# Kernel tuning notes

Hardware: AMD Instinct MI355X
Metric: run time of the kernel (lower is better)

## Reference

```python
import jax, jax.numpy as jnp
import numpy as np

B, S, H = 512, 50, 20
N_NODE, N_CAT = 100000, 1298
MEM, CLUS = 20, 10
STEP, KBLOCKS = 1, 2
MIX = 0.52  # a = 0.52*attn_last + 0.48*ht


def setup_inputs() -> dict:
    key = jax.random.key(0)
    ks = iter(jax.random.split(key, 48))
    stdv = 1.0 / np.sqrt(H)
    def u(shape):
        return jax.random.uniform(next(ks), shape, jnp.float32, -stdv, stdv)
    inp = {}
    inp['inputs'] = jax.random.randint(next(ks), (B, S), 0, N_NODE, dtype=jnp.int32)
    inp['category'] = jax.random.randint(next(ks), (B, S), 0, N_CAT, dtype=jnp.int32)
    inp['A'] = jax.random.uniform(next(ks), (B, S, 2 * S), jnp.float32)
    inp['mask'] = jnp.ones((B, S), jnp.int32)
    # embeddings
    inp['emb'] = u((N_NODE, H)); inp['emb1'] = u((N_CAT, H))
    # GNN params
    inp['w_ih'] = u((3 * H, 2 * H)); inp['w_hh'] = u((3 * H, H))
    inp['b_ih'] = u((3 * H,)); inp['b_hh'] = u((3 * H,))
    inp['b_iah'] = u((H,)); inp['b_oah'] = u((H,))
    inp['w_ein'] = u((H, H)); inp['b_ein'] = u((H,))
    inp['w_eout'] = u((H, H)); inp['b_eout'] = u((H,))
    # two single-head MHAs
    for p in ('mha', 'mha1'):
        inp[p + '_in_w'] = u((3 * H, H)); inp[p + '_in_b'] = u((3 * H,))
        inp[p + '_out_w'] = u((H, H)); inp[p + '_out_b'] = u((H,))
    # residual blocks
    for p in ('rn', 'rn1'):
        inp[p + '_w1'] = u((H, H)); inp[p + '_b1'] = u((H,))
        inp[p + '_w2'] = u((H, H)); inp[p + '_b2'] = u((H,))
    # memory readout
    inp['mem_M'] = u((CLUS, MEM)); inp['mem_Wa'] = u((2 * H, MEM)); inp['mem_fc'] = u((MEM, MEM))
    # heads
    inp['wc'] = u((H, 3 * H)); inp['bc'] = u((H,))
    inp['wp'] = u((H, 3 * H)); inp['bp'] = u((H,))
    return inp


def _mha(x, w_in, b_in, w_out, b_out):
    # Faithful to torch nn.MultiheadAttention (seq-first, 1 head):
    # x is [B,S,H] but torch treats dim0 as sequence -> attention mixes along axis 0.
    E = x.shape[-1]
    q, k, v = jnp.split(x @ w_in.T + b_in, 3, axis=-1)
    q = q * (1.0 / jnp.sqrt(jnp.float32(E)))
    scores = jnp.einsum('lne,mne->nlm', q, k)        # [S_axis1, L, L]
    attn = jax.nn.softmax(scores, axis=-1)
    out = jnp.einsum('nlm,mne->lne', attn, v)
    return out @ w_out.T + b_out


def _residual(x, w1, b1, w2, b2):
    # eval mode: dropout = identity
    return x + jax.nn.relu(x @ w1.T + b1) @ w2.T + b2


def _gnn_cell(A, h, w_ein, b_ein, w_eout, b_eout, b_iah, b_oah, w_ih, b_ih, w_hh, b_hh):
    s = h.shape[1]
    inp_in = jnp.einsum('bij,bjh->bih', A[:, :, :s], h @ w_ein.T + b_ein) + b_iah
    inp_out = jnp.einsum('bij,bjh->bih', A[:, :, s:2 * s], h @ w_eout.T + b_eout) + b_oah
    gi = jnp.concatenate([inp_in, inp_out], -1) @ w_ih.T + b_ih
    gh = h @ w_hh.T + b_hh
    i_r, i_i, i_n = jnp.split(gi, 3, -1)
    h_r, h_i, h_n = jnp.split(gh, 3, -1)
    r = jax.nn.sigmoid(i_r + h_r)
    z = jax.nn.sigmoid(i_i + h_i)
    n = jnp.tanh(i_n + r * h_n)
    return n + z * (h - n)


def reference(inputs, category, A, mask, emb, emb1, w_ih, w_hh, b_ih, b_hh, b_iah, b_oah,
              w_ein, b_ein, w_eout, b_eout,
              mha_in_w, mha_in_b, mha_out_w, mha_out_b,
              mha1_in_w, mha1_in_b, mha1_out_w, mha1_out_b,
              rn_w1, rn_b1, rn_w2, rn_b2, rn1_w1, rn1_b1, rn1_w2, rn1_b2,
              mem_M, mem_Wa, mem_fc, wc, bc, wp, bp):
    item_h = emb[inputs]          # [B,S,H]
    cat_h = emb1[category]        # [B,S,H]
    for _ in range(STEP):
        item_h = _gnn_cell(A, item_h, w_ein, b_ein, w_eout, b_eout,
                           b_iah, b_oah, w_ih, b_ih, w_hh, b_hh)
    bidx = jnp.arange(mask.shape[0])
    last = jnp.sum(mask, 1) - 1
    ht_item = item_h[bidx, last]
    ht_cat = cat_h[bidx, last]
    x = item_h
    for _ in range(KBLOCKS):
        x = _residual(_mha(x, mha_in_w, mha_in_b, mha_out_w, mha_out_b), rn_w1, rn_b1, rn_w2, rn_b2)
    a_item = MIX * x[bidx, last] + (1 - MIX) * ht_item
    y = cat_h
    for _ in range(KBLOCKS):
        y = _residual(_mha(y, mha1_in_w, mha1_in_b, mha1_out_w, mha1_out_b), rn1_w1, rn1_b1, rn1_w2, rn1_b2)
    a_cat = MIX * y[bidx, last] + (1 - MIX) * ht_cat
    a = jnp.concatenate([a_item, a_cat], -1)                # [B, 2H]
    att = jax.nn.softmax((a @ mem_Wa) @ mem_M.T, axis=-1)   # [B, CLUS]
    reps = jnp.tanh((att @ mem_M) @ mem_fc)                 # [B, MEM]
    car = jnp.concatenate([a, reps], -1)                    # [B, 3H]
    final = jax.nn.sigmoid(car @ wc.T + bc) * (car @ wp.T + bp)
    scores = final @ emb[1:].T                              # [B, N_NODE-1]
    return scores
```

## Files before the change

### kernel.cpp

```cpp
#include <hip/hip_runtime.h>
#include <hip/hip_bf16.h>

#define BB 512
#define SS 50
#define HH 20
#define NN 100000
#define MC 128
#define MT 16
#define PBSTRIDE ((size_t)BB*24)

__device__ __forceinline__ float frcp(float x){
#if __has_builtin(__builtin_amdgcn_rcpf)
  return __builtin_amdgcn_rcpf(x);
#else
  return 1.f/x;
#endif
}
__device__ __forceinline__ float fsig(float x){ return frcp(1.f + __expf(-x)); }
__device__ __forceinline__ float ftanh(float x){ return 1.f - 2.f*frcp(1.f + __expf(2.f*x)); }

__global__ __launch_bounds__(256)
void k_gnnqkv(const int* __restrict__ inputs, const int* __restrict__ category,
              const float* __restrict__ A, const int* __restrict__ mask,
              const float* __restrict__ emb, const float* __restrict__ emb1,
              const float* __restrict__ w_ih, const float* __restrict__ w_hh,
              const float* __restrict__ b_ih, const float* __restrict__ b_hh,
              const float* __restrict__ b_iah, const float* __restrict__ b_oah,
              const float* __restrict__ w_ein, const float* __restrict__ b_ein,
              const float* __restrict__ w_eout, const float* __restrict__ b_eout,
              const float* __restrict__ inw0, const float* __restrict__ inb0,
              const float* __restrict__ inw1, const float* __restrict__ inb1,
              float* __restrict__ q_t, float* __restrict__ k_t, float* __restrict__ v_t,
              int* __restrict__ last, float* __restrict__ ht_item, float* __restrict__ ht_cat)
{
    __shared__ float sA[SS*2*SS];
    __shared__ float sit[SS*HH], sct[SS*HH], shin[SS*HH], shout[SS*HH];
    __shared__ float sinp[SS*HH], soutp[SS*HH];
    __shared__ float swein[HH*HH], sweout[HH*HH];
    __shared__ float swih[60*40], swhh[60*HH];
    __shared__ float sw0[60*HH], sw1w[60*HH];
    __shared__ float sbein[HH], sbeout[HH], sbih[60], sbhh[60], sbiah[HH], sboah[HH], sb0[60], sb1b[60];
    __shared__ int slast;
    const int b = blockIdx.x, t = threadIdx.x;

    for (int i=t;i<SS*2*SS;i+=256) sA[i] = A[(size_t)b*SS*2*SS + i];
    for (int i=t;i<HH*HH;i+=256) { swein[i]=w_ein[i]; sweout[i]=w_eout[i]; }
    for (int i=t;i<60*40;i+=256) swih[i]=w_ih[i];
    for (int i=t;i<60*HH;i+=256) { swhh[i]=w_hh[i]; sw0[i]=inw0[i]; sw1w[i]=inw1[i]; }
    if (t<60){ sbih[t]=b_ih[t]; sbhh[t]=b_hh[t]; sb0[t]=inb0[t]; sb1b[t]=inb1[t]; }
    if (t<HH){ sbein[t]=b_ein[t]; sbeout[t]=b_eout[t]; sbiah[t]=b_iah[t]; sboah[t]=b_oah[t]; }
    for (int i=t;i<SS*HH;i+=256){
        int r=i/HH, e=i%HH;
        sit[i]=emb [(size_t)inputs  [b*SS+r]*HH+e];
        sct[i]=emb1[(size_t)category[b*SS+r]*HH+e];
    }
    if (t==0){ int s=0; for (int j=0;j<SS;j++) s+=mask[b*SS+j]; slast=s-1; }
    __syncthreads();

    for (int i=t;i<SS*HH;i+=256){
        int r=i/HH, c=i%HH;
        float si=sbein[c], so=sbeout[c];
        #pragma unroll
        for (int e=0;e<HH;e++){ float hv=sit[r*HH+e]; si+=swein[c*HH+e]*hv; so+=sweout[c*HH+e]*hv; }
        shin[i]=si; shout[i]=so;
    }
    __syncthreads();
    for (int i=t;i<SS*HH;i+=256){
        int r=i/HH, e=i%HH;
        float ai=sbiah[e], ao=sboah[e];
        for (int j=0;j<SS;j++){
            ai+=sA[r*2*SS+j]   *shin [j*HH+e];
            ao+=sA[r*2*SS+SS+j]*shout[j*HH+e];
        }
        sinp[i]=ai; soutp[i]=ao;
    }
    __syncthreads();
    float nh[4];
    #pragma unroll
    for (int ii=0;ii<4;ii++){
        int i=t+ii*256;
        if (i<SS*HH){
            int r=i/HH, e=i%HH;
            float gir=sbih[e], gii=sbih[20+e], gin=sbih[40+e];
            #pragma unroll
            for (int k=0;k<HH;k++){
                float vi=sinp[r*HH+k], vo=soutp[r*HH+k];
                gir+=swih[e*40+k]*vi      + swih[e*40+HH+k]*vo;
                gii+=swih[(20+e)*40+k]*vi + swih[(20+e)*40+HH+k]*vo;
                gin+=swih[(40+e)*40+k]*vi + swih[(40+e)*40+HH+k]*vo;
            }
            float ghr=sbhh[e], ghi=sbhh[20+e], ghn=sbhh[40+e];
            #pragma unroll
            for (int k=0;k<HH;k++){
                float hv=sit[r*HH+k];
                ghr+=swhh[e*HH+k]*hv; ghi+=swhh[(20+e)*HH+k]*hv; ghn+=swhh[(40+e)*HH+k]*hv;
            }
            float rr=fsig(gir+ghr), zz=fsig(gii+ghi);
            float nn2=ftanh(gin+rr*ghn);
            nh[ii]=nn2+zz*(sit[i]-nn2);
        }
    }
    __syncthreads();
    #pragma unroll
    for (int ii=0;ii<4;ii++){ int i=t+ii*256; if (i<SS*HH) sit[i]=nh[ii]; }
    __syncthreads();

    if (t<HH)                    ht_item[b*HH+t]      = sit[slast*HH+t];
    else if (t>=32 && t<32+HH)   ht_cat [b*HH+(t-32)] = sct[slast*HH+(t-32)];
    else if (t==63)              last[b]=slast;

    const float SCALE = 0.22360679774997896f;
    for (int oi=t; oi<2*SS*60; oi+=256){
        int p=oi/(SS*60); int rem=oi%(SS*60); int r=rem/60; int c=rem%60;
        const float* src = p? sct  : sit;
        const float* w   = p? sw1w : sw0;
        const float* bb_ = p? sb1b : sb0;
        float acc=bb_[c];
        #pragma unroll
        for (int e=0;e<HH;e++) acc += w[c*HH+e]*src[r*HH+e];
        int which=c/HH, cc=c%HH;
        size_t off=((size_t)(p*SS+r)*BB + b)*HH + cc;
        if (which==0)      q_t[off]=acc*SCALE;
        else if (which==1) k_t[off]=acc;
        else               v_t[off]=acc;
    }
}

__global__ __launch_bounds__(256)
void k_attn(const float* __restrict__ q_t, const float* __restrict__ k_t,
            const float* __restrict__ v_t, float* __restrict__ pbuf)
{
    __shared__ float sk[MC*HH], sv[MC*HH];
    const int n=blockIdx.x, p=blockIdx.y, mc=blockIdx.z, t=threadIdx.x;
    const size_t base=(size_t)(p*SS+n)*BB;
    {
        const float4* kb=(const float4*)(k_t+(base+(size_t)mc*MC)*HH);
        const float4* vb=(const float4*)(v_t+(base+(size_t)mc*MC)*HH);
        float4* sk4=(float4*)sk; float4* sv4=(float4*)sv;
        for (int i=t;i<MC*HH/4;i+=256){ sk4[i]=kb[i]; sv4[i]=vb[i]; }
    }
    __syncthreads();
    float4 q0[5], q1[5];
    {
        const float4* qp0=(const float4*)(q_t+(base+t)*HH);
        const float4* qp1=(const float4*)(q_t+(base+t+256)*HH);
        #pragma unroll
        for (int i=0;i<5;i++){ q0[i]=qp0[i]; q1[i]=qp1[i]; }
    }
    float4 o0[5], o1[5];
    #pragma unroll
    for (int i=0;i<5;i++){ o0[i]=make_float4(0.f,0.f,0.f,0.f); o1[i]=make_float4(0.f,0.f,0.f,0.f); }
    float mx0=-1e30f, mx1=-1e30f, sm0=0.f, sm1=0.f;

    for (int mt0=0; mt0<MC; mt0+=MT){
        float s0[MT], s1[MT];
        float tm0=-1e30f, tm1=-1e30f;
        #pragma unroll
        for (int j=0;j<MT;j++){
            const float4* kr=(const float4*)(sk+(mt0+j)*HH);
            float a0=0.f, a1=0.f;
            #pragma unroll
            for (int i=0;i<5;i++){
                float4 kv=kr[i];
                a0+=q0[i].x*kv.x+q0[i].y*kv.y+q0[i].z*kv.z+q0[i].w*kv.w;
                a1+=q1[i].x*kv.x+q1[i].y*kv.y+q1[i].z*kv.z+q1[i].w*kv.w;
            }
            s0[j]=a0; s1[j]=a1;
            tm0=fmaxf(tm0,a0); tm1=fmaxf(tm1,a1);
        }
        float nm0=fmaxf(mx0,tm0), nm1=fmaxf(mx1,tm1);
        float c0=__expf(mx0-nm0), c1=__expf(mx1-nm1);
        sm0*=c0; sm1*=c1;
        #pragma unroll
        for (int i=0;i<5;i++){
            o0[i].x*=c0; o0[i].y*=c0; o0[i].z*=c0; o0[i].w*=c0;
            o1[i].x*=c1; o1[i].y*=c1; o1[i].z*=c1; o1[i].w*=c1;
        }
        mx0=nm0; mx1=nm1;
        #pragma unroll
        for (int j=0;j<MT;j++){
            float p0=__expf(s0[j]-nm0), p1=__expf(s1[j]-nm1);
            sm0+=p0; sm1+=p1;
            const float4* vr=(const float4*)(sv+(mt0+j)*HH);
            #pragma unroll
            for (int i=0;i<5;i++){
                float4 vv=vr[i];
                o0[i].x+=p0*vv.x; o0[i].y+=p0*vv.y; o0[i].z+=p0*vv.z; o0[i].w+=p0*vv.w;
                o1[i].x+=p1*vv.x; o1[i].y+=p1*vv.y; o1[i].z+=p1*vv.z; o1[i].w+=p1*vv.w;
            }
        }
    }
    float* pb0 = pbuf + (((size_t)(p*SS+n)*4+mc)*BB + t)*24;
    float4* w0=(float4*)pb0;
    w0[0]=make_float4(mx0,sm0,o0[0].x,o0[0].y);
    w0[1]=make_float4(o0[0].z,o0[0].w,o0[1].x,o0[1].y);
    w0[2]=make_float4(o0[1].z,o0[1].w,o0[2].x,o0[2].y);
    w0[3]=make_float4(o0[2].z,o0[2].w,o0[3].x,o0[3].y);
    w0[4]=make_float4(o0[3].z,o0[3].w,o0[4].x,o0[4].y);
    w0[5]=make_float4(o0[4].z,o0[4].w,0.f,0.f);
    float4* w1=(float4*)(pb0 + (size_t)256*24);
    w1[0]=make_float4(mx1,sm1,o1[0].x,o1[0].y);
    w1[1]=make_float4(o1[0].z,o1[0].w,o1[1].x,o1[1].y);
    w1[2]=make_float4(o1[1].z,o1[1].w,o1[2].x,o1[2].y);
    w1[3]=make_float4(o1[2].z,o1[2].w,o1[3].x,o1[3].y);
    w1[4]=make_float4(o1[3].z,o1[3].w,o1[4].x,o1[4].y);
    w1[5]=make_float4(o1[4].z,o1[4].w,0.f,0.f);
}

__device__ __forceinline__ void merge_res(const float* __restrict__ pbase,
    const float* __restrict__ sow, const float* __restrict__ sob,
    const float* __restrict__ sw1, const float* __restrict__ sb1,
    const float* __restrict__ sw2, const float* __restrict__ sb2,
    float* __restrict__ xo)
{
    float mx=-1e30f;
    #pragma unroll
    for (int mc2=0;mc2<4;mc2++) mx=fmaxf(mx, pbase[mc2*PBSTRIDE]);
    float sum=0.f, o[HH];
    #pragma unroll
    for (int e=0;e<HH;e++) o[e]=0.f;
    #pragma unroll
    for (int mc2=0;mc2<4;mc2++){
        const float4* pc=(const float4*)(pbase+mc2*PBSTRIDE);
        float4 a=pc[0], b4=pc[1], c4=pc[2], d4=pc[3], e4=pc[4], f4=pc[5];
        float cc=__expf(a.x-mx);
        sum+=a.y*cc;
        o[0]+=a.z*cc;  o[1]+=a.w*cc;
        o[2]+=b4.x*cc; o[3]+=b4.y*cc; o[4]+=b4.z*cc; o[5]+=b4.w*cc;
        o[6]+=c4.x*cc; o[7]+=c4.y*cc; o[8]+=c4.z*cc; o[9]+=c4.w*cc;
        o[10]+=d4.x*cc; o[11]+=d4.y*cc; o[12]+=d4.z*cc; o[13]+=d4.w*cc;
        o[14]+=e4.x*cc; o[15]+=e4.y*cc; o[16]+=e4.z*cc; o[17]+=e4.w*cc;
        o[18]+=f4.x*cc; o[19]+=f4.y*cc;
    }
    float inv=frcp(sum);
    float ao[HH];
    #pragma unroll
    for (int e=0;e<HH;e++) ao[e]=o[e]*inv;
    float mo[HH];
    #pragma unroll
    for (int e=0;e<HH;e++){
        float acc=sob[e];
        #pragma unroll
        for (int f=0;f<HH;f++) acc+=sow[e*HH+f]*ao[f];
        mo[e]=acc;
    }
    float u[HH];
    #pragma unroll
    for (int g=0;g<HH;g++){
        float acc=sb1[g];
        #pragma unroll
        for (int f=0;f<HH;f++) acc+=sw1[g*HH+f]*mo[f];
        u[g]=fmaxf(acc,0.f);
    }
    #pragma unroll
    for (int e=0;e<HH;e++){
        float acc=mo[e]+sb2[e];
        #pragma unroll
        for (int g=0;g<HH;g++) acc+=sw2[e*HH+g]*u[g];
        xo[e]=acc;
    }
}

__global__ __launch_bounds__(256)
void k_finqkv(const float* __restrict__ pbuf,
    const float* __restrict__ ow0, const float* __restrict__ ob0,
    const float* __restrict__ w10, const float* __restrict__ b10,
    const float* __restrict__ w20, const float* __restrict__ b20,
    const float* __restrict__ iw0, const float* __restrict__ ib0,
    const float* __restrict__ ow1, const float* __restrict__ ob1,
    const float* __restrict__ w11, const float* __restrict__ b11,
    const float* __restrict__ w21, const float* __restrict__ b21,
    const float* __restrict__ iw1, const float* __restrict__ ib1,
    float* __restrict__ q_t, float* __restrict__ k_t, float* __restrict__ v_t)
{
    __shared__ float sow[400], sw1[400], sw2[400], siw[1200];
    __shared__ float sob[20], sb1[20], sb2[20], sib[60];
    const int p=blockIdx.y, t=threadIdx.x;
    const int s=blockIdx.x>>1, b=(blockIdx.x&1)*256+t;
    const float* OW=p?ow1:ow0; const float* OB=p?ob1:ob0;
    const float* W1=p?w11:w10; const float* B1=p?b11:b10;
    const float* W2=p?w21:w20; const float* B2=p?b21:b20;
    const float* IW=p?iw1:iw0; const float* IB=p?ib1:ib0;
    for (int i=t;i<400;i+=256){ sow[i]=OW[i]; sw1[i]=W1[i]; sw2[i]=W2[i]; }
    for (int i=t;i<1200;i+=256) siw[i]=IW[i];
    if (t<20){ sob[t]=OB[t]; sb1[t]=B1[t]; sb2[t]=B2[t]; }
    if (t<60) sib[t]=IB[t];
    __syncthreads();
    const float* pbase = pbuf + (((size_t)(p*SS+s)*4)*BB + b)*24;
    float xo[HH];
    merge_res(pbase, sow,sob,sw1,sb1,sw2,sb2, xo);
    const float SCALE = 0.22360679774997896f;
    size_t off0=((size_t)(p*SS+s)*BB + b)*HH;
    #pragma unroll
    for (int c=0;c<HH;c++){
        float aq=sib[c], ak=sib[20+c], av=sib[40+c];
        #pragma unroll
        for (int e=0;e<HH;e++){ float xv=xo[e]; aq+=siw[c*HH+e]*xv; ak+=siw[(20+c)*HH+e]*xv; av+=siw[(40+c)*HH+e]*xv; }
        q_t[off0+c]=aq*SCALE; k_t[off0+c]=ak; v_t[off0+c]=av;
    }
}

__global__ __launch_bounds__(256)
void k_fin(const float* __restrict__ pbuf,
    const float* __restrict__ ow0, const float* __restrict__ ob0,
    const float* __restrict__ w10, const float* __restrict__ b10,
    const float* __restrict__ w20, const float* __restrict__ b20,
    const float* __restrict__ ow1, const float* __restrict__ ob1,
    const float* __restrict__ w11, const float* __restrict__ b11,
    const float* __restrict__ w21, const float* __restrict__ b21,
    float* __restrict__ xout)
{
    __shared__ float sow[400], sw1[400], sw2[400];
    __shared__ float sob[20], sb1[20], sb2[20];
    const int p=blockIdx.y, t=threadIdx.x;
    const int s=blockIdx.x>>1, b=(blockIdx.x&1)*256+t;
    const float* OW=p?ow1:ow0; const float* OB=p?ob1:ob0;
    const float* W1=p?w11:w10; const float* B1=p?b11:b10;
    const float* W2=p?w21:w20; const float* B2=p?b21:b20;
    for (int i=t;i<400;i+=256){ sow[i]=OW[i]; sw1[i]=W1[i]; sw2[i]=W2[i]; }
    if (t<20){ sob[t]=OB[t]; sb1[t]=B1[t]; sb2[t]=B2[t]; }
    __syncthreads();
    const float* pbase = pbuf + (((size_t)(p*SS+s)*4)*BB + b)*24;
    float xo[HH];
    merge_res(pbase, sow,sob,sw1,sb1,sw2,sb2, xo);
    size_t off=((size_t)(p*BB+b)*SS + s)*HH;
    #pragma unroll
    for (int e=0;e<HH;e++) xout[off+e]=xo[e];
}

__global__ __launch_bounds__(64)
void k_head(const float* __restrict__ xout, const int* __restrict__ last,
            const float* __restrict__ ht_item, const float* __restrict__ ht_cat,
            const float* __restrict__ mem_M, const float* __restrict__ mem_Wa,
            const float* __restrict__ mem_fc,
            const float* __restrict__ wc, const float* __restrict__ bc,
            const float* __restrict__ wp, const float* __restrict__ bp,
            float* __restrict__ final_)
{
    int b=blockIdx.x*64+threadIdx.x;
    if (b>=BB) return;
    int l=last[b];
    const float* xi = xout + ((size_t)(0*BB+b)*SS + l)*HH;
    const float* xc = xout + ((size_t)(1*BB+b)*SS + l)*HH;
    float a[40];
    #pragma unroll
    for (int e=0;e<HH;e++){
        a[e]    = 0.52f*xi[e] + 0.48f*ht_item[b*HH+e];
        a[20+e] = 0.52f*xc[e] + 0.48f*ht_cat [b*HH+e];
    }
    float t20[20];
    #pragma unroll
    for (int j=0;j<20;j++){
        float acc=0.f;
        #pragma unroll
        for (int k=0;k<40;k++) acc+=a[k]*mem_Wa[k*20+j];
        t20[j]=acc;
    }
    float lg[10]; float mxv=-1e30f;
    #pragma unroll
    for (int c=0;c<10;c++){
        float acc=0.f;
        #pragma unroll
        for (int j=0;j<20;j++) acc+=t20[j]*mem_M[c*20+j];
        lg[c]=acc; mxv=fmaxf(mxv,acc);
    }
    float se=0.f;
    #pragma unroll
    for (int c=0;c<10;c++){ lg[c]=__expf(lg[c]-mxv); se+=lg[c]; }
    float inv=frcp(se);
    #pragma unroll
    for (int c=0;c<10;c++) lg[c]*=inv;
    float am[20];
    #pragma unroll
    for (int j=0;j<20;j++){
        float acc=0.f;
        #pragma unroll
        for (int c=0;c<10;c++) acc+=lg[c]*mem_M[c*20+j];
        am[j]=acc;
    }
    float reps[20];
    #pragma unroll
    for (int j2=0;j2<20;j2++){
        float acc=0.f;
        #pragma unroll
        for (int j=0;j<20;j++) acc+=am[j]*mem_fc[j*20+j2];
        reps[j2]=ftanh(acc);
    }
    #pragma unroll
    for (int e=0;e<HH;e++){
        float c1=bc[e], c2=bp[e];
        #pragma unroll
        for (int k=0;k<40;k++){ c1+=a[k]*wc[e*60+k]; c2+=a[k]*wp[e*60+k]; }
        #pragma unroll
        for (int k=0;k<20;k++){ c1+=reps[k]*wc[e*60+40+k]; c2+=reps[k]*wp[e*60+40+k]; }
        final_[b*HH+e]=fsig(c1)*c2;
    }
}

__global__ __launch_bounds__(256)
void k_scores(const float* __restrict__ final_, const float* __restrict__ emb,
              float* __restrict__ out)
{
    int node = blockIdx.x*256 + threadIdx.x;
    if (node >= NN-1) return;
    float4 er[5];
    const float4* e4 = (const float4*)(emb + ((size_t)node + 1)*HH);
    #pragma unroll
    for (int i=0;i<5;i++) er[i]=e4[i];
    float* op = out + node;
    for (int b = 0; b < BB; b++) {
        const float4* fb = (const float4*)(final_ + b*HH);
        float acc = 0.f;
        #pragma unroll
        for (int i=0;i<5;i++){
            float4 f=fb[i];
            acc += f.x*er[i].x + f.y*er[i].y + f.z*er[i].z + f.w*er[i].w;
        }
        *op = acc;
        op += (NN-1);
    }
}

extern "C" void kernel_launch(void* const* d_in, const int* in_sizes, int n_in,
                              void* d_out, int out_size, void* d_ws, size_t ws_size,
                              hipStream_t stream) {
    const int*   inputs   = (const int*)  d_in[0];
    const int*   category = (const int*)  d_in[1];
    const float* A        = (const float*)d_in[2];
    const int*   mask     = (const int*)  d_in[3];
    const float* emb      = (const float*)d_in[4];
    const float* emb1     = (const float*)d_in[5];
    const float* w_ih     = (const float*)d_in[6];
    const float* w_hh     = (const float*)d_in[7];
    const float* b_ih     = (const float*)d_in[8];
    const float* b_hh     = (const float*)d_in[9];
    const float* b_iah    = (const float*)d_in[10];
    const float* b_oah    = (const float*)d_in[11];
    const float* w_ein    = (const float*)d_in[12];
    const float* b_ein    = (const float*)d_in[13];
    const float* w_eout   = (const float*)d_in[14];
    const float* b_eout   = (const float*)d_in[15];
    const float* mha_in_w  = (const float*)d_in[16];
    const float* mha_in_b  = (const float*)d_in[17];
    const float* mha_out_w = (const float*)d_in[18];
    const float* mha_out_b = (const float*)d_in[19];
    const float* mha1_in_w  = (const float*)d_in[20];
    const float* mha1_in_b  = (const float*)d_in[21];
    const float* mha1_out_w = (const float*)d_in[22];
    const float* mha1_out_b = (const float*)d_in[23];
    const float* rn_w1 = (const float*)d_in[24];
    const float* rn_b1 = (const float*)d_in[25];
    const float* rn_w2 = (const float*)d_in[26];
    const float* rn_b2 = (const float*)d_in[27];
    const float* rn1_w1 = (const float*)d_in[28];
    const float* rn1_b1 = (const float*)d_in[29];
    const float* rn1_w2 = (const float*)d_in[30];
    const float* rn1_b2 = (const float*)d_in[31];
    const float* mem_M  = (const float*)d_in[32];
    const float* mem_Wa = (const float*)d_in[33];
    const float* mem_fc = (const float*)d_in[34];
    const float* wc = (const float*)d_in[35];
    const float* bc = (const float*)d_in[36];
    const float* wp = (const float*)d_in[37];
    const float* bp = (const float*)d_in[38];
    float* out = (float*)d_out;

    float* W = (float*)d_ws;
    float* q_t   = W;
    float* k_t   = W + 1024000;
    float* v_t   = W + 2048000;
    float* pbuf  = W + 3072000;
    float* xout  = W + 7987200;
    float* ht_item = W + 9011200;
    float* ht_cat  = W + 9021440;
    float* final_  = W + 9031680;
    int*   last    = (int*)(W + 9041920);

    k_gnnqkv<<<BB, 256, 0, stream>>>(inputs, category, A, mask, emb, emb1,
                                     w_ih, w_hh, b_ih, b_hh, b_iah, b_oah,
                                     w_ein, b_ein, w_eout, b_eout,
                                     mha_in_w, mha_in_b, mha1_in_w, mha1_in_b,
                                     q_t, k_t, v_t, last, ht_item, ht_cat);
    k_attn<<<dim3(SS,2,4), 256, 0, stream>>>(q_t, k_t, v_t, pbuf);
    k_finqkv<<<dim3(100,2), 256, 0, stream>>>(pbuf,
        mha_out_w, mha_out_b, rn_w1, rn_b1, rn_w2, rn_b2, mha_in_w, mha_in_b,
        mha1_out_w, mha1_out_b, rn1_w1, rn1_b1, rn1_w2, rn1_b2, mha1_in_w, mha1_in_b,
        q_t, k_t, v_t);
    k_attn<<<dim3(SS,2,4), 256, 0, stream>>>(q_t, k_t, v_t, pbuf);
    k_fin<<<dim3(100,2), 256, 0, stream>>>(pbuf,
        mha_out_w, mha_out_b, rn_w1, rn_b1, rn_w2, rn_b2,
        mha1_out_w, mha1_out_b, rn1_w1, rn1_b1, rn1_w2, rn1_b2,
        xout);
    k_head<<<8, 64, 0, stream>>>(xout, last, ht_item, ht_cat,
                                 mem_M, mem_Wa, mem_fc, wc, bc, wp, bp, final_);
    k_scores<<<(NN-1+255)/256, 256, 0, stream>>>(final_, emb, out);
}
```

Baseline: 656.1 us.

## Skip attention and residual work for sequence positions not used by any last index

A small kernel marks which sequence positions are some batch row's last index. Because attention mixes only along the batch axis, each position's output depends only on that same position. Attention, the intermediate residual/QKV kernel and the final kernel now return early for unmarked positions, and the final kernel writes only the mixed last-position vectors that the head needs. Attention is also split into more, smaller blocks (8 key chunks by 4 row chunks at 128 threads), which doubles the partial buffer and merge cost, and one GNN loop gets an unroll hint.

```diff
diff --git a/kernel.cpp b/kernel.cpp
--- a/kernel.cpp
+++ b/kernel.cpp
@@ -5,7 +5,9 @@
 #define SS 50
 #define HH 20
 #define NN 100000
-#define MC 128
+#define NMC 8
+#define MCH 64
+#define NRC 4
 #define MT 16
 #define PBSTRIDE ((size_t)BB*24)
 
@@ -68,6 +70,7 @@
     for (int i=t;i<SS*HH;i+=256){
         int r=i/HH, e=i%HH;
         float ai=sbiah[e], ao=sboah[e];
+        #pragma unroll 5
         for (int j=0;j<SS;j++){
             ai+=sA[r*2*SS+j]   *shin [j*HH+e];
             ao+=sA[r*2*SS+SS+j]*shout[j*HH+e];
@@ -127,84 +130,85 @@
 }
 
 __global__ __launch_bounds__(256)
+void k_flags(const int* __restrict__ last, int* __restrict__ needed)
+{
+    __shared__ int nf[SS];
+    int t=threadIdx.x;
+    if (t<SS) nf[t]=0;
+    __syncthreads();
+    for (int b=t;b<BB;b+=256){ int l=last[b]; atomicOr(&nf[l],1); }
+    __syncthreads();
+    if (t<SS) needed[t]=nf[t];
+}
+
+__global__ __launch_bounds__(128)
 void k_attn(const float* __restrict__ q_t, const float* __restrict__ k_t,
-            const float* __restrict__ v_t, float* __restrict__ pbuf)
-{
-    __shared__ float sk[MC*HH], sv[MC*HH];
-    const int n=blockIdx.x, p=blockIdx.y, mc=blockIdx.z, t=threadIdx.x;
-    const size_t base=(size_t)(p*SS+n)*BB;
+            const float* __restrict__ v_t, const int* __restrict__ needed,
+            float* __restrict__ pbuf)
+{
+    const int s=blockIdx.x, p=blockIdx.y, z=blockIdx.z;
+    if (!needed[s]) return;
+    const int mc=z>>2, rc=z&3, t=threadIdx.x;
+    __shared__ float sk[MCH*HH], sv[MCH*HH];
+    const size_t base=(size_t)(p*SS+s)*BB;
     {
-        const float4* kb=(const float4*)(k_t+(base+(size_t)mc*MC)*HH);
-        const float4* vb=(const float4*)(v_t+(base+(size_t)mc*MC)*HH);
+        const float4* kb=(const float4*)(k_t+(base+(size_t)mc*MCH)*HH);
+        const float4* vb=(const float4*)(v_t+(base+(size_t)mc*MCH)*HH);
         float4* sk4=(float4*)sk; float4* sv4=(float4*)sv;
-        for (int i=t;i<MC*HH/4;i+=256){ sk4[i]=kb[i]; sv4[i]=vb[i]; }
-    }
-    __syncthreads();
-    float4 q0[5], q1[5];
+        for (int i=t;i<MCH*HH/4;i+=128){ sk4[i]=kb[i]; sv4[i]=vb[i]; }
+    }
+    __syncthreads();
+    const int row = rc*128 + t;
+    float4 q[5];
     {
-        const float4* qp0=(const float4*)(q_t+(base+t)*HH);
-        const float4* qp1=(const float4*)(q_t+(base+t+256)*HH);
-        #pragma unroll
-        for (int i=0;i<5;i++){ q0[i]=qp0[i]; q1[i]=qp1[i]; }
-    }
-    float4 o0[5], o1[5];
-    #pragma unroll
-    for (int i=0;i<5;i++){ o0[i]=make_float4(0.f,0.f,0.f,0.f); o1[i]=make_float4(0.f,0.f,0.f,0.f); }
-    float mx0=-1e30f, mx1=-1e30f, sm0=0.f, sm1=0.f;
-
-    for (int mt0=0; mt0<MC; mt0+=MT){
-        float s0[MT], s1[MT];
-        float tm0=-1e30f, tm1=-1e30f;
+        const float4* qp=(const float4*)(q_t+(base+row)*HH);
+        #pragma unroll
+        for (int i=0;i<5;i++) q[i]=qp[i];
+    }
+    float4 o[5];
+    #pragma unroll
+    for (int i=0;i<5;i++) o[i]=make_float4(0.f,0.f,0.f,0.f);
+    float mx=-1e30f, sm=0.f;
+
+    for (int mt0=0; mt0<MCH; mt0+=MT){
+        float sc[MT]; float tm=-1e30f;
         #pragma unroll
         for (int j=0;j<MT;j++){
             const float4* kr=(const float4*)(sk+(mt0+j)*HH);
-            float a0=0.f, a1=0.f;
+            float a0=0.f;
             #pragma unroll
             for (int i=0;i<5;i++){
                 float4 kv=kr[i];
-                a0+=q0[i].x*kv.x+q0[i].y*kv.y+q0[i].z*kv.z+q0[i].w*kv.w;
-                a1+=q1[i].x*kv.x+q1[i].y*kv.y+q1[i].z*kv.z+q1[i].w*kv.w;
+                a0+=q[i].x*kv.x+q[i].y*kv.y+q[i].z*kv.z+q[i].w*kv.w;
             }
-            s0[j]=a0; s1[j]=a1;
-            tm0=fmaxf(tm0,a0); tm1=fmaxf(tm1,a1);
+            sc[j]=a0; tm=fmaxf(tm,a0);
         }
-        float nm0=fmaxf(mx0,tm0), nm1=fmaxf(mx1,tm1);
-        float c0=__expf(mx0-nm0), c1=__expf(mx1-nm1);
-        sm0*=c0; sm1*=c1;
-        #pragma unroll
-        for (int i=0;i<5;i++){
-            o0[i].x*=c0; o0[i].y*=c0; o0[i].z*=c0; o0[i].w*=c0;
-            o1[i].x*=c1; o1[i].y*=c1; o1[i].z*=c1; o1[i].w*=c1;
-        }
-        mx0=nm0; mx1=nm1;
+        float nm=fmaxf(mx,tm);
+        float c=__expf(mx-nm);
+        sm*=c;
+        #pragma unroll
+        for (int i=0;i<5;i++){ o[i].x*=c; o[i].y*=c; o[i].z*=c; o[i].w*=c; }
+        mx=nm;
         #pragma unroll
         for (int j=0;j<MT;j++){
-            float p0=__expf(s0[j]-nm0), p1=__expf(s1[j]-nm1);
-            sm0+=p0; sm1+=p1;
+            float pe=__expf(sc[j]-nm);
+            sm+=pe;
             const float4* vr=(const float4*)(sv+(mt0+j)*HH);
             #pragma unroll
             for (int i=0;i<5;i++){
                 float4 vv=vr[i];
-                o0[i].x+=p0*vv.x; o0[i].y+=p0*vv.y; o0[i].z+=p0*vv.z; o0[i].w+=p0*vv.w;
-                o1[i].x+=p1*vv.x; o1[i].y+=p1*vv.y; o1[i].z+=p1*vv.z; o1[i].w+=p1*vv.w;
+                o[i].x+=pe*vv.x; o[i].y+=pe*vv.y; o[i].z+=pe*vv.z; o[i].w+=pe*vv.w;
             }
         }
     }
-    float* pb0 = pbuf + (((size_t)(p*SS+n)*4+mc)*BB + t)*24;
-    float4* w0=(float4*)pb0;
-    w0[0]=make_float4(mx0,sm0,o0[0].x,o0[0].y);
-    w0[1]=make_float4(o0[0].z,o0[0].w,o0[1].x,o0[1].y);
-    w0[2]=make_float4(o0[1].z,o0[1].w,o0[2].x,o0[2].y);
-    w0[3]=make_float4(o0[2].z,o0[2].w,o0[3].x,o0[3].y);
-    w0[4]=make_float4(o0[3].z,o0[3].w,o0[4].x,o0[4].y);
-    w0[5]=make_float4(o0[4].z,o0[4].w,0.f,0.f);
-    float4* w1=(float4*)(pb0 + (size_t)256*24);
-    w1[0]=make_float4(mx1,sm1,o1[0].x,o1[0].y);
-    w1[1]=make_float4(o1[0].z,o1[0].w,o1[1].x,o1[1].y);
-    w1[2]=make_float4(o1[1].z,o1[1].w,o1[2].x,o1[2].y);
-    w1[3]=make_float4(o1[2].z,o1[2].w,o1[3].x,o1[3].y);
-    w1[4]=make_float4(o1[3].z,o1[3].w,o1[4].x,o1[4].y);
-    w1[5]=make_float4(o1[4].z,o1[4].w,0.f,0.f);
+    float* pb = pbuf + (((size_t)(p*SS+s)*NMC+mc)*BB + row)*24;
+    float4* w0=(float4*)pb;
+    w0[0]=make_float4(mx,sm,o[0].x,o[0].y);
+    w0[1]=make_float4(o[0].z,o[0].w,o[1].x,o[1].y);
+    w0[2]=make_float4(o[1].z,o[1].w,o[2].x,o[2].y);
+    w0[3]=make_float4(o[2].z,o[2].w,o[3].x,o[3].y);
+    w0[4]=make_float4(o[3].z,o[3].w,o[4].x,o[4].y);
+    w0[5]=make_float4(o[4].z,o[4].w,0.f,0.f);
 }
 
 __device__ __forceinline__ void merge_res(const float* __restrict__ pbase,
@@ -215,12 +219,12 @@
 {
     float mx=-1e30f;
     #pragma unroll
-    for (int mc2=0;mc2<4;mc2++) mx=fmaxf(mx, pbase[mc2*PBSTRIDE]);
+    for (int mc2=0;mc2<NMC;mc2++) mx=fmaxf(mx, pbase[mc2*PBSTRIDE]);
     float sum=0.f, o[HH];
     #pragma unroll
     for (int e=0;e<HH;e++) o[e]=0.f;
     #pragma unroll
-    for (int mc2=0;mc2<4;mc2++){
+    for (int mc2=0;mc2<NMC;mc2++){
         const float4* pc=(const float4*)(pbase+mc2*PBSTRIDE);
         float4 a=pc[0], b4=pc[1], c4=pc[2], d4=pc[3], e4=pc[4], f4=pc[5];
         float cc=__expf(a.x-mx);
@@ -262,7 +266,7 @@
 }
 
 __global__ __launch_bounds__(256)
-void k_finqkv(const float* __restrict__ pbuf,
+void k_finqkv(const float* __restrict__ pbuf, const int* __restrict__ needed,
     const float* __restrict__ ow0, const float* __restrict__ ob0,
     const float* __restrict__ w10, const float* __restrict__ b10,
     const float* __restrict__ w20, const float* __restrict__ b20,
@@ -273,10 +277,12 @@
     const float* __restrict__ iw1, const float* __restrict__ ib1,
     float* __restrict__ q_t, float* __restrict__ k_t, float* __restrict__ v_t)
 {
+    const int s=blockIdx.x>>1;
+    if (!needed[s]) return;
     __shared__ float sow[400], sw1[400], sw2[400], siw[1200];
     __shared__ float sob[20], sb1[20], sb2[20], sib[60];
     const int p=blockIdx.y, t=threadIdx.x;
-    const int s=blockIdx.x>>1, b=(blockIdx.x&1)*256+t;
+    const int b=(blockIdx.x&1)*256+t;
     const float* OW=p?ow1:ow0; const float* OB=p?ob1:ob0;
     const float* W1=p?w11:w10; const float* B1=p?b11:b10;
     const float* W2=p?w21:w20; const float* B2=p?b21:b20;
@@ -286,7 +292,7 @@
     if (t<20){ sob[t]=OB[t]; sb1[t]=B1[t]; sb2[t]=B2[t]; }
     if (t<60) sib[t]=IB[t];
     __syncthreads();
-    const float* pbase = pbuf + (((size_t)(p*SS+s)*4)*BB + b)*24;
+    const float* pbase = pbuf + (((size_t)(p*SS+s)*NMC)*BB + b)*24;
     float xo[HH];
     merge_res(pbase, sow,sob,sw1,sb1,sw2,sb2, xo);
     const float SCALE = 0.22360679774997896f;
@@ -301,36 +307,41 @@
 }
 
 __global__ __launch_bounds__(256)
-void k_fin(const float* __restrict__ pbuf,
+void k_fin(const float* __restrict__ pbuf, const int* __restrict__ needed,
+    const int* __restrict__ last,
+    const float* __restrict__ ht_item, const float* __restrict__ ht_cat,
     const float* __restrict__ ow0, const float* __restrict__ ob0,
     const float* __restrict__ w10, const float* __restrict__ b10,
     const float* __restrict__ w20, const float* __restrict__ b20,
     const float* __restrict__ ow1, const float* __restrict__ ob1,
     const float* __restrict__ w11, const float* __restrict__ b11,
     const float* __restrict__ w21, const float* __restrict__ b21,
-    float* __restrict__ xout)
-{
+    float* __restrict__ a_out)
+{
+    const int s=blockIdx.x>>1;
+    if (!needed[s]) return;
     __shared__ float sow[400], sw1[400], sw2[400];
     __shared__ float sob[20], sb1[20], sb2[20];
     const int p=blockIdx.y, t=threadIdx.x;
-    const int s=blockIdx.x>>1, b=(blockIdx.x&1)*256+t;
+    const int b=(blockIdx.x&1)*256+t;
     const float* OW=p?ow1:ow0; const float* OB=p?ob1:ob0;
     const float* W1=p?w11:w10; const float* B1=p?b11:b10;
     const float* W2=p?w21:w20; const float* B2=p?b21:b20;
     for (int i=t;i<400;i+=256){ sow[i]=OW[i]; sw1[i]=W1[i]; sw2[i]=W2[i]; }
     if (t<20){ sob[t]=OB[t]; sb1[t]=B1[t]; sb2[t]=B2[t]; }
     __syncthreads();
-    const float* pbase = pbuf + (((size_t)(p*SS+s)*4)*BB + b)*24;
+    if (last[b] != s) return;
+    const float* pbase = pbuf + (((size_t)(p*SS+s)*NMC)*BB + b)*24;
     float xo[HH];
     merge_res(pbase, sow,sob,sw1,sb1,sw2,sb2, xo);
-    size_t off=((size_t)(p*BB+b)*SS + s)*HH;
-    #pragma unroll
-    for (int e=0;e<HH;e++) xout[off+e]=xo[e];
+    const float* ht = p? ht_cat : ht_item;
+    #pragma unroll
+    for (int e=0;e<HH;e++)
+        a_out[(size_t)b*40 + p*HH + e] = 0.52f*xo[e] + 0.48f*ht[b*HH+e];
 }
 
 __global__ __launch_bounds__(64)
-void k_head(const float* __restrict__ xout, const int* __restrict__ last,
-            const float* __restrict__ ht_item, const float* __restrict__ ht_cat,
+void k_head(const float* __restrict__ a_in,
             const float* __restrict__ mem_M, const float* __restrict__ mem_Wa,
             const float* __restrict__ mem_fc,
             const float* __restrict__ wc, const float* __restrict__ bc,
@@ -339,15 +350,10 @@
 {
     int b=blockIdx.x*64+threadIdx.x;
     if (b>=BB) return;
-    int l=last[b];
-    const float* xi = xout + ((size_t)(0*BB+b)*SS + l)*HH;
-    const float* xc = xout + ((size_t)(1*BB+b)*SS + l)*HH;
     float a[40];
-    #pragma unroll
-    for (int e=0;e<HH;e++){
-        a[e]    = 0.52f*xi[e] + 0.48f*ht_item[b*HH+e];
-        a[20+e] = 0.52f*xc[e] + 0.48f*ht_cat [b*HH+e];
-    }
+    const float4* a4=(const float4*)(a_in+(size_t)b*40);
+    #pragma unroll
+    for (int i=0;i<10;i++){ float4 v=a4[i]; a[4*i]=v.x; a[4*i+1]=v.y; a[4*i+2]=v.z; a[4*i+3]=v.w; }
     float t20[20];
     #pragma unroll
     for (int j=0;j<20;j++){
@@ -466,32 +472,33 @@
     float* out = (float*)d_out;
 
     float* W = (float*)d_ws;
-    float* q_t   = W;
-    float* k_t   = W + 1024000;
-    float* v_t   = W + 2048000;
-    float* pbuf  = W + 3072000;
-    float* xout  = W + 7987200;
-    float* ht_item = W + 9011200;
-    float* ht_cat  = W + 9021440;
-    float* final_  = W + 9031680;
-    int*   last    = (int*)(W + 9041920);
+    float* q_t     = W;
+    float* k_t     = W + 1024000;
+    float* v_t     = W + 2048000;
+    float* pbuf    = W + 3072000;
+    float* ht_item = W + 12902400;
+    float* ht_cat  = W + 12912640;
+    float* a_buf   = W + 12922880;
+    float* final_  = W + 12943360;
+    int*   last    = (int*)(W + 12953600);
+    int*   needed  = (int*)(W + 12954112);
 
     k_gnnqkv<<<BB, 256, 0, stream>>>(inputs, category, A, mask, emb, emb1,
                                      w_ih, w_hh, b_ih, b_hh, b_iah, b_oah,
                                      w_ein, b_ein, w_eout, b_eout,
                                      mha_in_w, mha_in_b, mha1_in_w, mha1_in_b,
                                      q_t, k_t, v_t, last, ht_item, ht_cat);
-    k_attn<<<dim3(SS,2,4), 256, 0, stream>>>(q_t, k_t, v_t, pbuf);
-    k_finqkv<<<dim3(100,2), 256, 0, stream>>>(pbuf,
+    k_flags<<<1, 256, 0, stream>>>(last, needed);
+    k_attn<<<dim3(SS,2,NMC*NRC), 128, 0, stream>>>(q_t, k_t, v_t, needed, pbuf);
+    k_finqkv<<<dim3(100,2), 256, 0, stream>>>(pbuf, needed,
         mha_out_w, mha_out_b, rn_w1, rn_b1, rn_w2, rn_b2, mha_in_w, mha_in_b,
         mha1_out_w, mha1_out_b, rn1_w1, rn1_b1, rn1_w2, rn1_b2, mha1_in_w, mha1_in_b,
         q_t, k_t, v_t);
-    k_attn<<<dim3(SS,2,4), 256, 0, stream>>>(q_t, k_t, v_t, pbuf);
-    k_fin<<<dim3(100,2), 256, 0, stream>>>(pbuf,
+    k_attn<<<dim3(SS,2,NMC*NRC), 128, 0, stream>>>(q_t, k_t, v_t, needed, pbuf);
+    k_fin<<<dim3(100,2), 256, 0, stream>>>(pbuf, needed, last, ht_item, ht_cat,
         mha_out_w, mha_out_b, rn_w1, rn_b1, rn_w2, rn_b2,
         mha1_out_w, mha1_out_b, rn1_w1, rn1_b1, rn1_w2, rn1_b2,
-        xout);
-    k_head<<<8, 64, 0, stream>>>(xout, last, ht_item, ht_cat,
-                                 mem_M, mem_Wa, mem_fc, wc, bc, wp, bp, final_);
+        a_buf);
+    k_head<<<8, 64, 0, stream>>>(a_buf, mem_M, mem_Wa, mem_fc, wc, bc, wp, bp, final_);
     k_scores<<<(NN-1+255)/256, 256, 0, stream>>>(final_, emb, out);
 }
```

After: 582.7 us. 1.13x faster.
